# Kernel tuning notes

Measured on AMD Instinct MI355X. Metric: run time of the kernel, lower is better.

## Reference

```python
import jax, jax.numpy as jnp
import numpy as np

D_MODEL = 1024
N_HEADS = 16
D_K = D_MODEL // N_HEADS


def setup_inputs() -> dict:
    key = jax.random.key(0)
    ks = jax.random.split(key, 11)
    B, S = 2, 2048
    s = 1.0 / np.sqrt(D_MODEL)
    inp = {
        'query': jax.random.normal(ks[0], (B, S, D_MODEL), jnp.float32),
        'key': jax.random.normal(ks[1], (B, S, D_MODEL), jnp.float32),
        'value': jax.random.normal(ks[2], (B, S, D_MODEL), jnp.float32),
        'Wq': jax.random.normal(ks[3], (D_MODEL, D_MODEL), jnp.float32) * s,
        'bq': jnp.zeros((D_MODEL,), jnp.float32),
        'Wk': jax.random.normal(ks[4], (D_MODEL, D_MODEL), jnp.float32) * s,
        'bk': jnp.zeros((D_MODEL,), jnp.float32),
        'Wv': jax.random.normal(ks[5], (D_MODEL, D_MODEL), jnp.float32) * s,
        'bv': jnp.zeros((D_MODEL,), jnp.float32),
        'Wo': jax.random.normal(ks[6], (D_MODEL, D_MODEL), jnp.float32) * s,
        'bo': jnp.zeros((D_MODEL,), jnp.float32),
    }
    return inp


def reference(query, key, value, Wq, bq, Wk, bk, Wv, bv, Wo, bo):
    B, S, _ = query.shape
    # torch Linear: x @ W.T + b
    Q = query @ Wq.T + bq
    K = key @ Wk.T + bk
    V = value @ Wv.T + bv
    # [B, H, S, d_k]
    Q = Q.reshape(B, S, N_HEADS, D_K).transpose(0, 2, 1, 3)
    K = K.reshape(B, S, N_HEADS, D_K).transpose(0, 2, 1, 3)
    V = V.reshape(B, S, N_HEADS, D_K).transpose(0, 2, 1, 3)
    scores = jnp.einsum('bhqd,bhkd->bhqk', Q, K) / jnp.sqrt(jnp.float32(D_K))
    attn_weights = jax.nn.softmax(scores, axis=-1)
    context = jnp.einsum('bhqk,bhkd->bhqd', attn_weights, V)
    context = context.transpose(0, 2, 1, 3).reshape(B, S, N_HEADS * D_K)
    output = context @ Wo.T + bo
    return (output, attn_weights)
```

## Files before the change

kernel.cpp:

```cpp
#include <hip/hip_runtime.h>
#include <math.h>

#define BATCH   2
#define SEQ     2048
#define DMODEL  1024
#define NHEADS  16
#define DK      64
#define MROWS   (BATCH * SEQ)
#define OUT0_ELEMS ((size_t)BATCH * SEQ * DMODEL)

typedef _Float16 f16;
typedef _Float16 f16x8 __attribute__((ext_vector_type(8)));
typedef _Float16 f16x4 __attribute__((ext_vector_type(4)));
typedef float    f32x4 __attribute__((ext_vector_type(4)));

#define MFMA(a,b,c) __builtin_amdgcn_mfma_f32_16x16x32_f16(a,b,c,0,0,0)

__device__ inline void gload16(const void* g, void* l)
{
    __builtin_amdgcn_global_load_lds((const __attribute__((address_space(1))) void*)g,
                                     (__attribute__((address_space(3))) void*)l,
                                     16, 0, 0);
}

__global__ __launch_bounds__(256) void cast_f32_f16(const float* __restrict__ w,
                                                    f16* __restrict__ o)
{
    int i = blockIdx.x * 256 + threadIdx.x;
    float4 v = ((const float4*)w)[i];
    f16x4 r = { (f16)v.x, (f16)v.y, (f16)v.z, (f16)v.w };
    ((f16x4*)o)[i] = r;
}

template<typename OT, int TRANSV>
__global__ __launch_bounds__(256) void gemm_tn(const f16* __restrict__ A,
                                               const f16* __restrict__ W16,
                                               const float* __restrict__ bias,
                                               OT* __restrict__ out)
{
    __shared__ f16 As[64 * 64];
    __shared__ f16 Bs[64 * 64];

    const int tid = threadIdx.x;
    const int w  = tid >> 6;
    const int l  = tid & 63;
    const int lr = l & 15;
    const int lg = l >> 4;
    const int m0 = blockIdx.x * 64;
    const int n0 = blockIdx.y * 64;
    const int wm = (w >> 1) * 32;
    const int wn = (w & 1) * 32;

    int srow[2], scol[2];
#pragma unroll
    for (int it = 0; it < 2; ++it) {
        int o = it * 4096 + tid * 16;
        int row = o >> 7;
        int slot = ((o >> 4) & 7) ^ (row & 7);
        srow[it] = row;
        scol[it] = slot * 8;
    }

    f32x4 acc[2][2] = {};

    for (int k0 = 0; k0 < DMODEL; k0 += 64) {
#pragma unroll
        for (int it = 0; it < 2; ++it) {
            gload16(A   + (size_t)(m0 + srow[it]) * DMODEL + k0 + scol[it],
                    (char*)As + it * 4096 + w * 1024);
            gload16(W16 + (size_t)(n0 + srow[it]) * DMODEL + k0 + scol[it],
                    (char*)Bs + it * 4096 + w * 1024);
        }
        __syncthreads();

        f16x8 af[2][2], bf[2][2];
#pragma unroll
        for (int kk = 0; kk < 2; ++kk)
#pragma unroll
            for (int i = 0; i < 2; ++i) {
                af[kk][i] = *(const f16x8*)((char*)As + (wm + i*16 + lr) * 128
                                            + (((kk*4 + lg) ^ (lr & 7)) << 4));
                bf[kk][i] = *(const f16x8*)((char*)Bs + (wn + i*16 + lr) * 128
                                            + (((kk*4 + lg) ^ (lr & 7)) << 4));
            }
#pragma unroll
        for (int kk = 0; kk < 2; ++kk)
#pragma unroll
            for (int i = 0; i < 2; ++i)
#pragma unroll
                for (int j = 0; j < 2; ++j)
                    acc[i][j] = MFMA(af[kk][i], bf[kk][j], acc[i][j]);
        __syncthreads();
    }

    float bv_[2];
#pragma unroll
    for (int j = 0; j < 2; ++j) bv_[j] = bias[n0 + wn + j*16 + lr];

#pragma unroll
    for (int i = 0; i < 2; ++i)
#pragma unroll
        for (int j = 0; j < 2; ++j)
#pragma unroll
            for (int r = 0; r < 4; ++r) {
                int row = m0 + wm + i*16 + lg*4 + r;
                int col = n0 + wn + j*16 + lr;
                float v = acc[i][j][r] + bv_[j];
                if constexpr (TRANSV)
                    out[((size_t)((row >> 11) * DMODEL + col)) * SEQ + (row & (SEQ-1))] = (OT)v;
                else
                    out[(size_t)row * DMODEL + col] = (OT)v;
            }
}

__global__ __launch_bounds__(512) void attn_kernel(const f16* __restrict__ Q16,
                                                   const f16* __restrict__ K16,
                                                   const f16* __restrict__ Vt16,
                                                   float* __restrict__ attnP,
                                                   f16* __restrict__ C16)
{
    __shared__ f16 Ps[8 * 1024];
    const int bh = blockIdx.x;
    const int qt = blockIdx.y;
    const int b  = bh >> 4, h = bh & 15;
    const int tid = threadIdx.x;
    const int w  = tid >> 6;
    const int l  = tid & 63;
    const int lr = l & 15;
    const int lg = l >> 4;
    const int q0 = qt * 128 + w * 16;

    char* ps = (char*)Ps + w * 2048;

    const f16* qp = Q16 + (size_t)(b*SEQ + q0 + lr) * DMODEL + h*DK + lg*8;
    f16x8 qf0 = *(const f16x8*)qp;
    f16x8 qf1 = *(const f16x8*)(qp + 32);

    const f16* kbase0 = K16 + (size_t)(b*SEQ) * DMODEL + h*DK + lg*8;

    float m_run = -INFINITY, l_run = 0.f;
    for (int kt = 0; kt < SEQ/64; ++kt) {
        f32x4 s[4] = {};
        const f16* kb = kbase0 + (size_t)(kt*64 + lr) * DMODEL;
#pragma unroll
        for (int j = 0; j < 4; ++j) {
            f16x8 kf0 = *(const f16x8*)(kb + (size_t)j*16*DMODEL);
            f16x8 kf1 = *(const f16x8*)(kb + (size_t)j*16*DMODEL + 32);
            s[j] = MFMA(kf0, qf0, s[j]);
            s[j] = MFMA(kf1, qf1, s[j]);
        }
        float mt = s[0][0];
#pragma unroll
        for (int j = 0; j < 4; ++j)
#pragma unroll
            for (int r = 0; r < 4; ++r) mt = fmaxf(mt, s[j][r]);
        mt = fmaxf(mt, __shfl_xor(mt, 16));
        mt = fmaxf(mt, __shfl_xor(mt, 32));
        float mn = fmaxf(m_run, mt);
        float se = 0.f;
#pragma unroll
        for (int j = 0; j < 4; ++j)
#pragma unroll
            for (int r = 0; r < 4; ++r) se += __expf((s[j][r] - mn) * 0.125f);
        se += __shfl_xor(se, 16);
        se += __shfl_xor(se, 32);
        l_run = l_run * __expf((m_run - mn) * 0.125f) + se;
        m_run = mn;
    }
    const float inv_l = 1.0f / l_run;

    f32x4 cacc[4] = {};
    const f16* vbase = Vt16 + (size_t)(b*DMODEL + h*DK + lr) * SEQ + lg*8;
    float* prow = attnP + ((size_t)bh*SEQ + q0 + lr) * SEQ;

    for (int kt = 0; kt < SEQ/64; ++kt) {
        f32x4 s[4] = {};
        const f16* kb = kbase0 + (size_t)(kt*64 + lr) * DMODEL;
#pragma unroll
        for (int j = 0; j < 4; ++j) {
            f16x8 kf0 = *(const f16x8*)(kb + (size_t)j*16*DMODEL);
            f16x8 kf1 = *(const f16x8*)(kb + (size_t)j*16*DMODEL + 32);
            s[j] = MFMA(kf0, qf0, s[j]);
            s[j] = MFMA(kf1, qf1, s[j]);
        }
#pragma unroll
        for (int j = 0; j < 4; ++j) {
            f32x4 p;
#pragma unroll
            for (int r = 0; r < 4; ++r)
                p[r] = __expf((s[j][r] - m_run) * 0.125f) * inv_l;
            *(float4*)(prow + kt*64 + j*16 + lg*4) = *(const float4*)&p;
            f16x4 ph = { (f16)p[0], (f16)p[1], (f16)p[2], (f16)p[3] };
            *(f16x4*)(ps + lr*128
                      + ((((j*2 + (lg >> 1)) ^ (lr & 7)) << 4) | ((lg & 1) << 3))) = ph;
        }
        asm volatile("s_waitcnt lgkmcnt(0)" ::: "memory");
        __builtin_amdgcn_sched_barrier(0);

        f16x8 pa0 = *(const f16x8*)(ps + lr*128 + (((lg    ) ^ (lr & 7)) << 4));
        f16x8 pa1 = *(const f16x8*)(ps + lr*128 + (((4 + lg) ^ (lr & 7)) << 4));

        const f16* vb = vbase + kt*64;
#pragma unroll
        for (int j = 0; j < 4; ++j) {
            f16x8 vf0 = *(const f16x8*)(vb + (size_t)j*16*SEQ);
            f16x8 vf1 = *(const f16x8*)(vb + (size_t)j*16*SEQ + 32);
            cacc[j] = MFMA(pa0, vf0, cacc[j]);
            cacc[j] = MFMA(pa1, vf1, cacc[j]);
        }
    }

#pragma unroll
    for (int j = 0; j < 4; ++j)
#pragma unroll
        for (int r = 0; r < 4; ++r) {
            int row = q0 + lg*4 + r;
            int col = h*DK + j*16 + lr;
            C16[(size_t)(b*SEQ + row) * DMODEL + col] = (f16)cacc[j][r];
        }
}

extern "C" void kernel_launch(void* const* d_in, const int* in_sizes, int n_in,
                              void* d_out, int out_size, void* d_ws, size_t ws_size,
                              hipStream_t stream)
{
    const float* query = (const float*)d_in[0];
    const float* key   = (const float*)d_in[1];
    const float* value = (const float*)d_in[2];
    const float* Wq    = (const float*)d_in[3];
    const float* bq    = (const float*)d_in[4];
    const float* Wk    = (const float*)d_in[5];
    const float* bk    = (const float*)d_in[6];
    const float* Wv    = (const float*)d_in[7];
    const float* bv    = (const float*)d_in[8];
    const float* Wo    = (const float*)d_in[9];
    const float* bo    = (const float*)d_in[10];

    float* out  = (float*)d_out;
    float* attn = (float*)d_out + OUT0_ELEMS;

    f16* Q16  = (f16*)d_ws;
    f16* K16  = Q16  + (size_t)MROWS * DMODEL;
    f16* Vt16 = K16  + (size_t)MROWS * DMODEL;
    f16* C16  = Vt16 + (size_t)MROWS * DMODEL;
    f16* Wq16 = C16  + (size_t)MROWS * DMODEL;
    f16* Wk16 = Wq16 + (size_t)DMODEL * DMODEL;
    f16* Wv16 = Wk16 + (size_t)DMODEL * DMODEL;
    f16* Wo16 = Wv16 + (size_t)DMODEL * DMODEL;
    f16* Xq   = Wo16 + (size_t)DMODEL * DMODEL;
    f16* Xk   = Xq   + (size_t)MROWS * DMODEL;
    f16* Xv   = Xk   + (size_t)MROWS * DMODEL;

    dim3 t256(256);
    hipLaunchKernelGGL(cast_f32_f16, dim3(1024), t256, 0, stream, Wq, Wq16);
    hipLaunchKernelGGL(cast_f32_f16, dim3(1024), t256, 0, stream, Wk, Wk16);
    hipLaunchKernelGGL(cast_f32_f16, dim3(1024), t256, 0, stream, Wv, Wv16);
    hipLaunchKernelGGL(cast_f32_f16, dim3(1024), t256, 0, stream, Wo, Wo16);
    hipLaunchKernelGGL(cast_f32_f16, dim3(4096), t256, 0, stream, query, Xq);
    hipLaunchKernelGGL(cast_f32_f16, dim3(4096), t256, 0, stream, key,   Xk);
    hipLaunchKernelGGL(cast_f32_f16, dim3(4096), t256, 0, stream, value, Xv);

    dim3 gProj(MROWS / 64, DMODEL / 64);
    hipLaunchKernelGGL((gemm_tn<f16, 0>),  gProj, t256, 0, stream, Xq, Wq16, bq, Q16);
    hipLaunchKernelGGL((gemm_tn<f16, 0>),  gProj, t256, 0, stream, Xk, Wk16, bk, K16);
    hipLaunchKernelGGL((gemm_tn<f16, 1>),  gProj, t256, 0, stream, Xv, Wv16, bv, Vt16);

    dim3 tAttn(512), gAttn(BATCH * NHEADS, SEQ / 128);
    hipLaunchKernelGGL(attn_kernel, gAttn, tAttn, 0, stream, Q16, K16, Vt16, attn, C16);

    hipLaunchKernelGGL((gemm_tn<float, 0>), gProj, t256, 0, stream, C16, Wo16, bo, out);
}
```

Measured before the change: 968.8 us.

## Use 128x128 GEMM tiles, separate V transpose, and prefetch K in attention

Projection GEMMs move to 128x128 tiles with 512 threads, and the f16 outputs are staged through LDS so they can be written as coalesced vector stores. The transposed V write leaves the GEMM epilogue and becomes its own LDS-tiled transpose kernel. The attention kernel uses 256-thread blocks with 64 queries each and double-buffers K fragments in registers to prefetch the next tile. It also folds 1/l into the exponent offset and writes the attention probabilities with nontemporal stores. Workspace buffers are reused, and the changes aim at global-memory access efficiency and latency hiding at the cost of an extra kernel launch and more register pressure.

After: 952.9 us. No clear change (-1.6%).

```diff
diff --git a/kernel.cpp b/kernel.cpp
--- a/kernel.cpp
+++ b/kernel.cpp
@@ -32,61 +32,64 @@
     ((f16x4*)o)[i] = r;
 }
 
-template<typename OT, int TRANSV>
-__global__ __launch_bounds__(256) void gemm_tn(const f16* __restrict__ A,
+template<typename OT>
+__global__ __launch_bounds__(512) void gemm128(const f16* __restrict__ A,
                                                const f16* __restrict__ W16,
                                                const float* __restrict__ bias,
                                                OT* __restrict__ out)
 {
-    __shared__ f16 As[64 * 64];
-    __shared__ f16 Bs[64 * 64];
+    __shared__ __align__(16) char lds[32768];
+    f16* As = (f16*)lds;
+    f16* Bs = (f16*)(lds + 16384);
 
     const int tid = threadIdx.x;
     const int w  = tid >> 6;
     const int l  = tid & 63;
     const int lr = l & 15;
     const int lg = l >> 4;
-    const int m0 = blockIdx.x * 64;
-    const int n0 = blockIdx.y * 64;
-    const int wm = (w >> 1) * 32;
-    const int wn = (w & 1) * 32;
+    const int m0 = blockIdx.x * 128;
+    const int n0 = blockIdx.y * 128;
+    const int wm = (w >> 2) * 64;
+    const int wn = (w & 3) * 32;
 
     int srow[2], scol[2];
 #pragma unroll
     for (int it = 0; it < 2; ++it) {
-        int o = it * 4096 + tid * 16;
+        int o = it * 8192 + tid * 16;
         int row = o >> 7;
         int slot = ((o >> 4) & 7) ^ (row & 7);
         srow[it] = row;
         scol[it] = slot * 8;
     }
 
-    f32x4 acc[2][2] = {};
+    f32x4 acc[4][2] = {};
 
     for (int k0 = 0; k0 < DMODEL; k0 += 64) {
 #pragma unroll
         for (int it = 0; it < 2; ++it) {
             gload16(A   + (size_t)(m0 + srow[it]) * DMODEL + k0 + scol[it],
-                    (char*)As + it * 4096 + w * 1024);
+                    (char*)As + it * 8192 + w * 1024);
             gload16(W16 + (size_t)(n0 + srow[it]) * DMODEL + k0 + scol[it],
-                    (char*)Bs + it * 4096 + w * 1024);
+                    (char*)Bs + it * 8192 + w * 1024);
         }
         __syncthreads();
 
-        f16x8 af[2][2], bf[2][2];
-#pragma unroll
-        for (int kk = 0; kk < 2; ++kk)
-#pragma unroll
-            for (int i = 0; i < 2; ++i) {
+        f16x8 af[2][4], bf[2][2];
+#pragma unroll
+        for (int kk = 0; kk < 2; ++kk) {
+#pragma unroll
+            for (int i = 0; i < 4; ++i)
                 af[kk][i] = *(const f16x8*)((char*)As + (wm + i*16 + lr) * 128
                                             + (((kk*4 + lg) ^ (lr & 7)) << 4));
-                bf[kk][i] = *(const f16x8*)((char*)Bs + (wn + i*16 + lr) * 128
+#pragma unroll
+            for (int j = 0; j < 2; ++j)
+                bf[kk][j] = *(const f16x8*)((char*)Bs + (wn + j*16 + lr) * 128
                                             + (((kk*4 + lg) ^ (lr & 7)) << 4));
-            }
+        }
 #pragma unroll
         for (int kk = 0; kk < 2; ++kk)
 #pragma unroll
-            for (int i = 0; i < 2; ++i)
+            for (int i = 0; i < 4; ++i)
 #pragma unroll
                 for (int j = 0; j < 2; ++j)
                     acc[i][j] = MFMA(af[kk][i], bf[kk][j], acc[i][j]);
@@ -97,29 +100,144 @@
 #pragma unroll
     for (int j = 0; j < 2; ++j) bv_[j] = bias[n0 + wn + j*16 + lr];
 
-#pragma unroll
-    for (int i = 0; i < 2; ++i)
-#pragma unroll
-        for (int j = 0; j < 2; ++j)
-#pragma unroll
-            for (int r = 0; r < 4; ++r) {
-                int row = m0 + wm + i*16 + lg*4 + r;
-                int col = n0 + wn + j*16 + lr;
-                float v = acc[i][j][r] + bv_[j];
-                if constexpr (TRANSV)
-                    out[((size_t)((row >> 11) * DMODEL + col)) * SEQ + (row & (SEQ-1))] = (OT)v;
-                else
-                    out[(size_t)row * DMODEL + col] = (OT)v;
-            }
-}
-
-__global__ __launch_bounds__(512) void attn_kernel(const f16* __restrict__ Q16,
-                                                   const f16* __restrict__ K16,
-                                                   const f16* __restrict__ Vt16,
-                                                   float* __restrict__ attnP,
-                                                   f16* __restrict__ C16)
-{
-    __shared__ f16 Ps[8 * 1024];
+    if constexpr (sizeof(OT) == 2) {
+        f16* Cs = (f16*)lds;
+#pragma unroll
+        for (int i = 0; i < 4; ++i)
+#pragma unroll
+            for (int j = 0; j < 2; ++j)
+#pragma unroll
+                for (int r = 0; r < 4; ++r)
+                    Cs[(wm + i*16 + lg*4 + r) * 128 + wn + j*16 + lr] =
+                        (f16)(acc[i][j][r] + bv_[j]);
+        __syncthreads();
+#pragma unroll
+        for (int p = 0; p < 4; ++p) {
+            int row = p*32 + (tid >> 4);
+            int c   = (tid & 15) * 8;
+            *(f16x8*)((f16*)out + (size_t)(m0 + row) * DMODEL + n0 + c) =
+                *(const f16x8*)&Cs[row * 128 + c];
+        }
+    } else {
+#pragma unroll
+        for (int i = 0; i < 4; ++i)
+#pragma unroll
+            for (int j = 0; j < 2; ++j)
+#pragma unroll
+                for (int r = 0; r < 4; ++r)
+                    out[(size_t)(m0 + wm + i*16 + lg*4 + r) * DMODEL
+                        + n0 + wn + j*16 + lr] = acc[i][j][r] + bv_[j];
+    }
+}
+
+__global__ __launch_bounds__(256) void transpose_v(const f16* __restrict__ V,
+                                                   f16* __restrict__ Vt)
+{
+    __shared__ f16 T[64][68];
+    const int bx = blockIdx.x;
+    const int b  = bx >> 5;
+    const int s0 = (bx & 31) * 64;
+    const int d0 = blockIdx.y * 64;
+    const int tid = threadIdx.x;
+
+#pragma unroll
+    for (int p = 0; p < 2; ++p) {
+        int s = p*32 + (tid >> 3);
+        int c = (tid & 7) * 8;
+        *(f16x8*)&T[s][c] = *(const f16x8*)(V + (size_t)(b*SEQ + s0 + s) * DMODEL + d0 + c);
+    }
+    __syncthreads();
+#pragma unroll
+    for (int p = 0; p < 2; ++p) {
+        int d  = p*32 + (tid >> 3);
+        int sc = (tid & 7) * 8;
+        f16x8 v;
+#pragma unroll
+        for (int e = 0; e < 8; ++e) v[e] = T[sc + e][d];
+        *(f16x8*)(Vt + (size_t)(b*DMODEL + d0 + d) * SEQ + s0 + sc) = v;
+    }
+}
+
+#define LOADK(B0, B1, ktv) do {                                                 \
+    const f16* kp_ = kbase0 + (size_t)((ktv)*64 + lr) * DMODEL;                 \
+    _Pragma("unroll")                                                           \
+    for (int j_ = 0; j_ < 4; ++j_) {                                            \
+        B0[j_] = *(const f16x8*)(kp_ + (size_t)j_*16*DMODEL);                   \
+        B1[j_] = *(const f16x8*)(kp_ + (size_t)j_*16*DMODEL + 32);              \
+    } } while (0)
+
+#define QK(B0, B1, s) do {                                                      \
+    _Pragma("unroll")                                                           \
+    for (int j_ = 0; j_ < 4; ++j_) {                                            \
+        s[j_] = MFMA(B0[j_], qf0, s[j_]);                                       \
+        s[j_] = MFMA(B1[j_], qf1, s[j_]);                                       \
+    } } while (0)
+
+#define P1BODY(C0, C1, N0, N1, ktv, PREF) do {                                  \
+    if (PREF) LOADK(N0, N1, (ktv)+1);                                           \
+    f32x4 s[4] = {};                                                            \
+    QK(C0, C1, s);                                                              \
+    float mt = s[0][0];                                                         \
+    _Pragma("unroll")                                                           \
+    for (int j_ = 0; j_ < 4; ++j_)                                              \
+        _Pragma("unroll")                                                       \
+        for (int r_ = 0; r_ < 4; ++r_) mt = fmaxf(mt, s[j_][r_]);               \
+    mt = fmaxf(mt, __shfl_xor(mt, 16));                                         \
+    mt = fmaxf(mt, __shfl_xor(mt, 32));                                         \
+    float mn = fmaxf(m_run, mt);                                                \
+    float mo_ = -mn * 0.125f;                                                   \
+    float se = 0.f;                                                             \
+    _Pragma("unroll")                                                           \
+    for (int j_ = 0; j_ < 4; ++j_)                                              \
+        _Pragma("unroll")                                                       \
+        for (int r_ = 0; r_ < 4; ++r_) se += __expf(fmaf(s[j_][r_], 0.125f, mo_)); \
+    se += __shfl_xor(se, 16);                                                   \
+    se += __shfl_xor(se, 32);                                                   \
+    l_run = l_run * __expf((m_run - mn) * 0.125f) + se;                         \
+    m_run = mn;                                                                 \
+    } while (0)
+
+#define P2BODY(C0, C1, N0, N1, ktv, PREF) do {                                  \
+    if (PREF) LOADK(N0, N1, (ktv)+1);                                           \
+    f16x8 vf0[4], vf1[4];                                                       \
+    {   const f16* vb_ = vbase + (ktv)*64;                                      \
+        _Pragma("unroll")                                                       \
+        for (int j_ = 0; j_ < 4; ++j_) {                                        \
+            vf0[j_] = *(const f16x8*)(vb_ + (size_t)j_*16*SEQ);                 \
+            vf1[j_] = *(const f16x8*)(vb_ + (size_t)j_*16*SEQ + 32);            \
+        } }                                                                     \
+    f32x4 s[4] = {};                                                            \
+    QK(C0, C1, s);                                                              \
+    _Pragma("unroll")                                                           \
+    for (int j_ = 0; j_ < 4; ++j_) {                                            \
+        f32x4 p_;                                                               \
+        _Pragma("unroll")                                                       \
+        for (int r_ = 0; r_ < 4; ++r_)                                          \
+            p_[r_] = __expf(fmaf(s[j_][r_], 0.125f, poff));                     \
+        __builtin_nontemporal_store(p_,                                         \
+            (f32x4*)(prow + (ktv)*64 + j_*16 + lg*4));                          \
+        f16x4 ph_ = { (f16)p_[0], (f16)p_[1], (f16)p_[2], (f16)p_[3] };         \
+        *(f16x4*)(ps + lr*128                                                   \
+            + ((((j_*2 + (lg >> 1)) ^ (lr & 7)) << 4) | ((lg & 1) << 3))) = ph_; \
+    }                                                                           \
+    asm volatile("s_waitcnt lgkmcnt(0)" ::: "memory");                          \
+    __builtin_amdgcn_sched_barrier(0);                                          \
+    {   f16x8 pa0_ = *(const f16x8*)(ps + lr*128 + (((lg    ) ^ (lr & 7)) << 4)); \
+        f16x8 pa1_ = *(const f16x8*)(ps + lr*128 + (((4 + lg) ^ (lr & 7)) << 4)); \
+        _Pragma("unroll")                                                       \
+        for (int j_ = 0; j_ < 4; ++j_) {                                        \
+            cacc[j_] = MFMA(pa0_, vf0[j_], cacc[j_]);                           \
+            cacc[j_] = MFMA(pa1_, vf1[j_], cacc[j_]);                           \
+        } }                                                                     \
+    } while (0)
+
+__global__ __launch_bounds__(256, 3) void attn_kernel(const f16* __restrict__ Q16,
+                                                      const f16* __restrict__ K16,
+                                                      const f16* __restrict__ Vt16,
+                                                      float* __restrict__ attnP,
+                                                      f16* __restrict__ C16)
+{
+    __shared__ f16 Ps[4 * 1024];
     const int bh = blockIdx.x;
     const int qt = blockIdx.y;
     const int b  = bh >> 4, h = bh & 15;
@@ -128,7 +246,7 @@
     const int l  = tid & 63;
     const int lr = l & 15;
     const int lg = l >> 4;
-    const int q0 = qt * 128 + w * 16;
+    const int q0 = qt * 64 + w * 16;
 
     char* ps = (char*)Ps + w * 2048;
 
@@ -137,78 +255,31 @@
     f16x8 qf1 = *(const f16x8*)(qp + 32);
 
     const f16* kbase0 = K16 + (size_t)(b*SEQ) * DMODEL + h*DK + lg*8;
+    const f16* vbase  = Vt16 + (size_t)(b*DMODEL + h*DK + lr) * SEQ + lg*8;
+
+    f16x8 kA0[4], kA1[4], kB0[4], kB1[4];
 
     float m_run = -INFINITY, l_run = 0.f;
-    for (int kt = 0; kt < SEQ/64; ++kt) {
-        f32x4 s[4] = {};
-        const f16* kb = kbase0 + (size_t)(kt*64 + lr) * DMODEL;
-#pragma unroll
-        for (int j = 0; j < 4; ++j) {
-            f16x8 kf0 = *(const f16x8*)(kb + (size_t)j*16*DMODEL);
-            f16x8 kf1 = *(const f16x8*)(kb + (size_t)j*16*DMODEL + 32);
-            s[j] = MFMA(kf0, qf0, s[j]);
-            s[j] = MFMA(kf1, qf1, s[j]);
-        }
-        float mt = s[0][0];
-#pragma unroll
-        for (int j = 0; j < 4; ++j)
-#pragma unroll
-            for (int r = 0; r < 4; ++r) mt = fmaxf(mt, s[j][r]);
-        mt = fmaxf(mt, __shfl_xor(mt, 16));
-        mt = fmaxf(mt, __shfl_xor(mt, 32));
-        float mn = fmaxf(m_run, mt);
-        float se = 0.f;
-#pragma unroll
-        for (int j = 0; j < 4; ++j)
-#pragma unroll
-            for (int r = 0; r < 4; ++r) se += __expf((s[j][r] - mn) * 0.125f);
-        se += __shfl_xor(se, 16);
-        se += __shfl_xor(se, 32);
-        l_run = l_run * __expf((m_run - mn) * 0.125f) + se;
-        m_run = mn;
-    }
-    const float inv_l = 1.0f / l_run;
+    LOADK(kA0, kA1, 0);
+    for (int kt = 0; kt < 30; kt += 2) {
+        P1BODY(kA0, kA1, kB0, kB1, kt,   1);
+        P1BODY(kB0, kB1, kA0, kA1, kt+1, 1);
+    }
+    P1BODY(kA0, kA1, kB0, kB1, 30, 1);
+    P1BODY(kB0, kB1, kA0, kA1, 31, 0);
+
+    const float poff = fmaf(m_run, -0.125f, -logf(l_run));
 
     f32x4 cacc[4] = {};
-    const f16* vbase = Vt16 + (size_t)(b*DMODEL + h*DK + lr) * SEQ + lg*8;
     float* prow = attnP + ((size_t)bh*SEQ + q0 + lr) * SEQ;
 
-    for (int kt = 0; kt < SEQ/64; ++kt) {
-        f32x4 s[4] = {};
-        const f16* kb = kbase0 + (size_t)(kt*64 + lr) * DMODEL;
-#pragma unroll
-        for (int j = 0; j < 4; ++j) {
-            f16x8 kf0 = *(const f16x8*)(kb + (size_t)j*16*DMODEL);
-            f16x8 kf1 = *(const f16x8*)(kb + (size_t)j*16*DMODEL + 32);
-            s[j] = MFMA(kf0, qf0, s[j]);
-            s[j] = MFMA(kf1, qf1, s[j]);
-        }
-#pragma unroll
-        for (int j = 0; j < 4; ++j) {
-            f32x4 p;
-#pragma unroll
-            for (int r = 0; r < 4; ++r)
-                p[r] = __expf((s[j][r] - m_run) * 0.125f) * inv_l;
-            *(float4*)(prow + kt*64 + j*16 + lg*4) = *(const float4*)&p;
-            f16x4 ph = { (f16)p[0], (f16)p[1], (f16)p[2], (f16)p[3] };
-            *(f16x4*)(ps + lr*128
-                      + ((((j*2 + (lg >> 1)) ^ (lr & 7)) << 4) | ((lg & 1) << 3))) = ph;
-        }
-        asm volatile("s_waitcnt lgkmcnt(0)" ::: "memory");
-        __builtin_amdgcn_sched_barrier(0);
-
-        f16x8 pa0 = *(const f16x8*)(ps + lr*128 + (((lg    ) ^ (lr & 7)) << 4));
-        f16x8 pa1 = *(const f16x8*)(ps + lr*128 + (((4 + lg) ^ (lr & 7)) << 4));
-
-        const f16* vb = vbase + kt*64;
-#pragma unroll
-        for (int j = 0; j < 4; ++j) {
-            f16x8 vf0 = *(const f16x8*)(vb + (size_t)j*16*SEQ);
-            f16x8 vf1 = *(const f16x8*)(vb + (size_t)j*16*SEQ + 32);
-            cacc[j] = MFMA(pa0, vf0, cacc[j]);
-            cacc[j] = MFMA(pa1, vf1, cacc[j]);
-        }
-    }
+    LOADK(kA0, kA1, 0);
+    for (int kt = 0; kt < 30; kt += 2) {
+        P2BODY(kA0, kA1, kB0, kB1, kt,   1);
+        P2BODY(kB0, kB1, kA0, kA1, kt+1, 1);
+    }
+    P2BODY(kA0, kA1, kB0, kB1, 30, 1);
+    P2BODY(kB0, kB1, kA0, kA1, 31, 0);
 
 #pragma unroll
     for (int j = 0; j < 4; ++j)
@@ -241,17 +312,18 @@
 
     f16* Q16  = (f16*)d_ws;
     f16* K16  = Q16  + (size_t)MROWS * DMODEL;
-    f16* Vt16 = K16  + (size_t)MROWS * DMODEL;
-    f16* C16  = Vt16 + (size_t)MROWS * DMODEL;
-    f16* Wq16 = C16  + (size_t)MROWS * DMODEL;
+    f16* V16  = K16  + (size_t)MROWS * DMODEL;
+    f16* Wq16 = V16  + (size_t)MROWS * DMODEL;
     f16* Wk16 = Wq16 + (size_t)DMODEL * DMODEL;
     f16* Wv16 = Wk16 + (size_t)DMODEL * DMODEL;
     f16* Wo16 = Wv16 + (size_t)DMODEL * DMODEL;
     f16* Xq   = Wo16 + (size_t)DMODEL * DMODEL;
     f16* Xk   = Xq   + (size_t)MROWS * DMODEL;
     f16* Xv   = Xk   + (size_t)MROWS * DMODEL;
-
-    dim3 t256(256);
+    f16* Vt16 = Xq;
+    f16* C16  = Xk;
+
+    dim3 t256(256), t512(512);
     hipLaunchKernelGGL(cast_f32_f16, dim3(1024), t256, 0, stream, Wq, Wq16);
     hipLaunchKernelGGL(cast_f32_f16, dim3(1024), t256, 0, stream, Wk, Wk16);
     hipLaunchKernelGGL(cast_f32_f16, dim3(1024), t256, 0, stream, Wv, Wv16);
@@ -260,13 +332,16 @@
     hipLaunchKernelGGL(cast_f32_f16, dim3(4096), t256, 0, stream, key,   Xk);
     hipLaunchKernelGGL(cast_f32_f16, dim3(4096), t256, 0, stream, value, Xv);
 
-    dim3 gProj(MROWS / 64, DMODEL / 64);
-    hipLaunchKernelGGL((gemm_tn<f16, 0>),  gProj, t256, 0, stream, Xq, Wq16, bq, Q16);
-    hipLaunchKernelGGL((gemm_tn<f16, 0>),  gProj, t256, 0, stream, Xk, Wk16, bk, K16);
-    hipLaunchKernelGGL((gemm_tn<f16, 1>),  gProj, t256, 0, stream, Xv, Wv16, bv, Vt16);
-
-    dim3 tAttn(512), gAttn(BATCH * NHEADS, SEQ / 128);
-    hipLaunchKernelGGL(attn_kernel, gAttn, tAttn, 0, stream, Q16, K16, Vt16, attn, C16);
-
-    hipLaunchKernelGGL((gemm_tn<float, 0>), gProj, t256, 0, stream, C16, Wo16, bo, out);
-}
+    dim3 gProj(MROWS / 128, DMODEL / 128);
+    hipLaunchKernelGGL((gemm128<f16>), gProj, t512, 0, stream, Xq, Wq16, bq, Q16);
+    hipLaunchKernelGGL((gemm128<f16>), gProj, t512, 0, stream, Xk, Wk16, bk, K16);
+    hipLaunchKernelGGL((gemm128<f16>), gProj, t512, 0, stream, Xv, Wv16, bv, V16);
+
+    dim3 gTr(MROWS / 64, DMODEL / 64);
+    hipLaunchKernelGGL(transpose_v, gTr, t256, 0, stream, V16, Vt16);
+
+    dim3 gAttn(BATCH * NHEADS, SEQ / 64);
+    hipLaunchKernelGGL(attn_kernel, gAttn, t256, 0, stream, Q16, K16, Vt16, attn, C16);
+
+    hipLaunchKernelGGL((gemm128<float>), gProj, t512, 0, stream, C16, Wo16, bo, out);
+}
```
